# Performance work log

Measured on AMD Instinct MI355X. Metric: run time of the kernel, lower is better.

Reference implementation:

```python
import jax, jax.numpy as jnp
import numpy as np
from jax import lax

B, T_IN, T_OUT = 32, 256, 500
N_MEL, ENC_DIM = 80, 512
ATT_RNN, DEC_RNN, PRENET, ATT_DIM = 1024, 1024, 256, 128
LOC_F, LOC_K = 32, 31
P_ATT_DROP, P_DEC_DROP = 0.1, 0.1


def setup_inputs() -> dict:
    key = jax.random.key(0)
    ks = jax.random.split(key, 24)
    rn = lambda k, s, sc=0.02: jax.random.normal(k, s, dtype=jnp.float32) * sc
    inp = {}
    inp['memory'] = jax.random.normal(ks[0], (B, T_IN, ENC_DIM), dtype=jnp.float32)
    inp['decoder_inputs'] = jax.random.normal(ks[1], (B, N_MEL, T_OUT), dtype=jnp.float32)
    inp['memory_lengths'] = jax.random.randint(ks[2], (B,), T_IN // 2, T_IN + 1)
    inp['prenet_w1'] = rn(ks[3], (PRENET, N_MEL))
    inp['prenet_w2'] = rn(ks[4], (PRENET, PRENET))
    inp['att_w_ih'] = rn(ks[5], (4 * ATT_RNN, PRENET + ENC_DIM))
    inp['att_w_hh'] = rn(ks[6], (4 * ATT_RNN, ATT_RNN))
    inp['att_b_ih'] = jnp.zeros((4 * ATT_RNN,), jnp.float32)
    inp['att_b_hh'] = jnp.zeros((4 * ATT_RNN,), jnp.float32)
    inp['query_w'] = rn(ks[7], (ATT_DIM, ATT_RNN))
    inp['memory_w'] = rn(ks[8], (ATT_DIM, ENC_DIM))
    inp['v_w'] = rn(ks[9], (1, ATT_DIM))
    inp['loc_conv_w'] = rn(ks[10], (LOC_F, 2, LOC_K))
    inp['loc_dense_w'] = rn(ks[11], (ATT_DIM, LOC_F))
    inp['dec_w_ih'] = rn(ks[12], (4 * DEC_RNN, ATT_RNN + ENC_DIM))
    inp['dec_w_hh'] = rn(ks[13], (4 * DEC_RNN, DEC_RNN))
    inp['dec_b_ih'] = jnp.zeros((4 * DEC_RNN,), jnp.float32)
    inp['dec_b_hh'] = jnp.zeros((4 * DEC_RNN,), jnp.float32)
    inp['proj_w'] = rn(ks[14], (N_MEL, DEC_RNN + ENC_DIM))
    inp['proj_b'] = jnp.zeros((N_MEL,), jnp.float32)
    inp['gate_w'] = rn(ks[15], (1, DEC_RNN + ENC_DIM))
    inp['gate_b'] = jnp.zeros((1,), jnp.float32)
    return inp


def _lstm_cell(x, h, c, w_ih, w_hh, b_ih, b_hh):
    gates = x @ w_ih.T + b_ih + h @ w_hh.T + b_hh
    i, f, g, o = jnp.split(gates, 4, axis=-1)
    c2 = jax.nn.sigmoid(f) * c + jax.nn.sigmoid(i) * jnp.tanh(g)
    h2 = jax.nn.sigmoid(o) * jnp.tanh(c2)
    return h2, c2


def _dropout_masks():
    # deterministic dropout masks (training=True semantics), keep-prob scaled
    kd = jax.random.key(1)
    k1, k2, k3, k4 = jax.random.split(kd, 4)
    m1 = jax.random.bernoulli(k1, 0.5, (T_OUT + 1, B, PRENET)).astype(jnp.float32) / 0.5
    m2 = jax.random.bernoulli(k2, 0.5, (T_OUT + 1, B, PRENET)).astype(jnp.float32) / 0.5
    ma = jax.random.bernoulli(k3, 1 - P_ATT_DROP, (T_OUT, B, ATT_RNN)).astype(jnp.float32) / (1 - P_ATT_DROP)
    md = jax.random.bernoulli(k4, 1 - P_DEC_DROP, (T_OUT, B, DEC_RNN)).astype(jnp.float32) / (1 - P_DEC_DROP)
    return m1, m2, ma, md


def _decode(memory, decoder_inputs, memory_lengths, prenet_w1, prenet_w2,
            att_w_ih, att_w_hh, att_b_ih, att_b_hh, query_w, memory_w, v_w,
            loc_conv_w, loc_dense_w, dec_w_ih, dec_w_hh, dec_b_ih, dec_b_hh,
            proj_w, proj_b, gate_w, gate_b):
    pm1, pm2, att_drop, dec_drop = _dropout_masks()
    processed_memory = jnp.einsum('bte,ae->bta', memory, memory_w)  # (B,T_in,128)
    pad_mask = jnp.arange(T_IN)[None, :] >= memory_lengths[:, None]  # True = padded

    # teacher-forced decoder inputs: (B,n_mel,T) -> (T,B,n_mel), prepend go frame
    dec_in = jnp.transpose(decoder_inputs, (2, 0, 1))
    dec_in = jnp.concatenate([jnp.zeros((1, B, N_MEL), dec_in.dtype), dec_in], 0)
    # prenet (relu + dropout p=0.5, always training)
    x = jax.nn.relu(dec_in @ prenet_w1.T) * pm1
    x = jax.nn.relu(x @ prenet_w2.T) * pm2
    prenet_out = x[:T_OUT]  # (T,B,256)

    pad = (LOC_K - 1) // 2

    def attention(att_h, aw, aw_cum):
        pq = att_h @ query_w.T  # (B,128)
        awc = jnp.stack([aw, aw_cum], axis=1)  # (B,2,T_in)
        loc = lax.conv_general_dilated(awc, loc_conv_w, (1,), [(pad, pad)],
                                       dimension_numbers=('NCH', 'OIH', 'NCH'))  # (B,32,T_in)
        loc = jnp.einsum('bft,af->bta', loc, loc_dense_w)  # (B,T_in,128)
        energies = jnp.tanh(pq[:, None, :] + loc + processed_memory) @ v_w[0]  # (B,T_in)
        energies = jnp.where(pad_mask, -jnp.inf, energies)
        w = jax.nn.softmax(energies, axis=1)
        ctx = jnp.einsum('bt,bte->be', w, memory)  # (B,512)
        return ctx, w

    def step(carry, xs):
        ah, ac, dh, dc, aw, aw_cum, ctx = carry
        pn, adm, ddm = xs
        cell_in = jnp.concatenate([pn, ctx], axis=-1)  # (B,768)
        ah, ac = _lstm_cell(cell_in, ah, ac, att_w_ih, att_w_hh, att_b_ih, att_b_hh)
        ah = ah * adm
        ctx, aw = attention(ah, aw, aw_cum)
        aw_cum = aw_cum + aw
        din = jnp.concatenate([ah, ctx], axis=-1)  # (B,1536)
        dh, dc = _lstm_cell(din, dh, dc, dec_w_ih, dec_w_hh, dec_b_ih, dec_b_hh)
        dh = dh * ddm
        dhac = jnp.concatenate([dh, ctx], axis=-1)  # (B,1536)
        mel = dhac @ proj_w.T + proj_b  # (B,80)
        gate = (dhac @ gate_w.T + gate_b)[:, 0]  # (B,)
        return (ah, ac, dh, dc, aw, aw_cum, ctx), (mel, gate, aw)

    z = lambda d: jnp.zeros((B, d), jnp.float32)
    init = (z(ATT_RNN), z(ATT_RNN), z(DEC_RNN), z(DEC_RNN),
            jnp.zeros((B, T_IN), jnp.float32), jnp.zeros((B, T_IN), jnp.float32), z(ENC_DIM))
    _, (mels, gates, aligns) = lax.scan(step, init, (prenet_out, att_drop, dec_drop))

    mel_outputs = jnp.transpose(mels, (1, 2, 0))   # (B, n_mel, T_out)
    gate_outputs = gates.T                          # (B, T_out)
    alignments = jnp.transpose(aligns, (1, 0, 2))   # (B, T_out, T_in)
    return mel_outputs, gate_outputs, alignments


def reference(memory, decoder_inputs, memory_lengths, prenet_w1, prenet_w2,
              att_w_ih, att_w_hh, att_b_ih, att_b_hh, query_w, memory_w, v_w,
              loc_conv_w, loc_dense_w, dec_w_ih, dec_w_hh, dec_b_ih, dec_b_hh,
              proj_w, proj_b, gate_w, gate_b):
    return _decode(memory, decoder_inputs, memory_lengths, prenet_w1, prenet_w2,
                   att_w_ih, att_w_hh, att_b_ih, att_b_hh, query_w, memory_w, v_w,
                   loc_conv_w, loc_dense_w, dec_w_ih, dec_w_hh, dec_b_ih, dec_b_hh,
                   proj_w, proj_b, gate_w, gate_b)
```

## Files before the change

kernel.cpp:

```cpp
#include <hip/hip_runtime.h>
#include <math.h>
#include <string.h>

#define TOUT 500
#define AOFF 1296000
#define GOFF 1280000
#define TF_BITS_XOR 1

typedef float f32x4 __attribute__((ext_vector_type(4)));
typedef short bf16x8 __attribute__((ext_vector_type(8)));
typedef unsigned short ushort4_t __attribute__((ext_vector_type(4)));
typedef unsigned u32x4 __attribute__((ext_vector_type(4)));

struct Params {
  const float *memory, *dec_in, *pw1, *pw2, *awih, *awhh, *abih, *abhh;
  const float *qw, *mw, *vw, *lcw, *ldw, *dwih, *dwhh, *dbih, *dbhh;
  const float *pjw, *pjb, *gw, *gb;
  const int* mlen;
  float* out;
  unsigned short *ahb0, *ahb1, *dhb0, *dhb1, *ctxb0, *ctxb1;
  unsigned *slots;
  unsigned *abf;
  unsigned *dbf;
  unsigned *attflag;
  unsigned *decflag;
  float *x1, *w1t, *w2t, *mwt, *ldwt, *ba, *bd;
  unsigned short *pre_bf, *pm_bf, *mem_t, *qw_bf, *wpa, *wpd;
  unsigned *mma, *mmd, *mm1, *mm2;
};

__host__ __device__ inline void tf_block(unsigned k0, unsigned k1, unsigned x0, unsigned x1,
                                         unsigned& o0, unsigned& o1) {
  unsigned ks2 = k0 ^ k1 ^ 0x1BD11BDAu;
  x0 += k0; x1 += k1;
#define TFR(r) { x0 += x1; x1 = (x1 << r) | (x1 >> (32 - r)); x1 ^= x0; }
  TFR(13) TFR(15) TFR(26) TFR(6)
  x0 += k1;  x1 += ks2 + 1u;
  TFR(17) TFR(29) TFR(16) TFR(24)
  x0 += ks2; x1 += k0 + 2u;
  TFR(13) TFR(15) TFR(26) TFR(6)
  x0 += k0;  x1 += k1 + 3u;
  TFR(17) TFR(29) TFR(16) TFR(24)
  x0 += k1;  x1 += ks2 + 4u;
  TFR(13) TFR(15) TFR(26) TFR(6)
  x0 += ks2; x1 += k0 + 5u;
#undef TFR
  o0 = x0; o1 = x1;
}

__device__ inline float sigf(float x) { return 1.f / (1.f + __expf(-x)); }
__device__ inline float tanh_fast(float x) {
  float ax = fabsf(x);
  float t = __expf(-2.f * ax);
  float r = (1.f - t) / (1.f + t);
  return copysignf(r, x);
}
__device__ inline unsigned short f2bf(float f) {
  unsigned u = __float_as_uint(f);
  unsigned r = (u + 0x7FFFu + ((u >> 16) & 1u)) >> 16;
  return (unsigned short)r;
}
__device__ inline float bf2f(unsigned short u) {
  return __uint_as_float((unsigned)u << 16);
}

__device__ inline unsigned long long ld_coh64(const void* ptr) {
  return __hip_atomic_load((unsigned long long*)ptr, __ATOMIC_RELAXED, __HIP_MEMORY_SCOPE_SYSTEM);
}
__device__ inline unsigned ld_coh32(const unsigned* ptr) {
  return __hip_atomic_load(ptr, __ATOMIC_RELAXED, __HIP_MEMORY_SCOPE_SYSTEM);
}
__device__ inline void st_coh32(unsigned* ptr, unsigned v) {
  __hip_atomic_store(ptr, v, __ATOMIC_RELAXED, __HIP_MEMORY_SCOPE_SYSTEM);
}

template<bool COH>
__device__ __forceinline__ u32x4 ld16(const void* ptr) {
  u32x4 r;
  if constexpr (COH)
    asm volatile("global_load_dwordx4 %0, %1, off sc0 sc1" : "=v"(r) : "v"(ptr));
  else
    asm volatile("global_load_dwordx4 %0, %1, off" : "=v"(r) : "v"(ptr));
  return r;
}

#define LD4(p) (*(const float4*)(p))

__global__ void maskgen_kernel(Params p, unsigned k1a, unsigned k1b, unsigned k2a, unsigned k2b,
                               unsigned k3a, unsigned k3b, unsigned k4a, unsigned k4b) {
  int t = blockIdx.x * 256 + threadIdx.x;
  unsigned ka, kb; unsigned* dst; float pp;
  if (t < 512000)       { ka = k3a; kb = k3b; dst = p.mma; pp = 0.9f; }
  else if (t < 1024000) { t -= 512000;  ka = k4a; kb = k4b; dst = p.mmd; pp = 0.9f; }
  else if (t < 1152256) { t -= 1024000; ka = k1a; kb = k1b; dst = p.mm1; pp = 0.5f; }
  else if (t < 1280512) { t -= 1152256; ka = k2a; kb = k2b; dst = p.mm2; pp = 0.5f; }
  else return;
  unsigned word = 0u;
  for (int i = 0; i < 32; ++i) {
    unsigned o0, o1;
    tf_block(ka, kb, 0u, (unsigned)t * 32u + (unsigned)i, o0, o1);
#if TF_BITS_XOR
    unsigned bits = o0 ^ o1;
#else
    unsigned bits = o0;
#endif
    unsigned fb = (bits >> 9) | 0x3f800000u;
    float u = __uint_as_float(fb) - 1.0f;
    if (u < pp) word |= (1u << i);
  }
  dst[t] = word;
}

__global__ void prep_misc(Params p) {
  int i = blockIdx.x * 256 + threadIdx.x;
  if (i < 20480) { int k = i >> 8, u = i & 255; p.w1t[i] = p.pw1[u * 80 + k]; return; }
  i -= 20480;
  if (i < 65536) { int k = i >> 8, u = i & 255; p.w2t[i] = p.pw2[u * 256 + k]; return; }
  i -= 65536;
  if (i < 65536) { int k = i >> 7, a = i & 127; p.mwt[i] = p.mw[a * 512 + k]; return; }
  i -= 65536;
  if (i < 131072) { p.qw_bf[i] = f2bf(p.qw[i]); return; }
  i -= 131072;
  if (i < 4096) { int f = i >> 7, a = i & 127; p.ldwt[i] = p.ldw[a * 32 + f]; return; }
  i -= 4096;
  if (i < 4096) { int col = (i & 3) * 1024 + (i >> 2); p.ba[i] = p.abih[col] + p.abhh[col]; return; }
  i -= 4096;
  if (i < 4096) { int col = (i & 3) * 1024 + (i >> 2); p.bd[i] = p.dbih[col] + p.dbhh[col]; return; }
  i -= 4096;
  if (i < 4194304) {
    int b = i >> 17, rem = i & 131071, d = rem >> 8, t = rem & 255;
    p.mem_t[i] = f2bf(p.memory[((size_t)b * 256 + t) * 512 + d]);
    return;
  }
}

__global__ void pack_att(Params p) {
  int idx = blockIdx.x * 256 + threadIdx.x;
  if (idx >= 256 * 56 * 64) return;
  int l = idx & 63;
  int c = (idx >> 6) % 56;
  int T = idx / (56 * 64);
  int n = T * 16 + (l & 15);
  int col = (n & 3) * 1024 + (n >> 2);
  int kb = c * 32 + 8 * (l >> 4);
  bf16x8 v;
#pragma unroll
  for (int j = 0; j < 8; ++j) {
    int k = kb + j;
    float f = (k < 768) ? p.awih[(size_t)col * 768 + k] : p.awhh[(size_t)col * 1024 + k - 768];
    v[j] = (short)f2bf(f);
  }
  *(bf16x8*)(p.wpa + (size_t)idx * 8) = v;
}
__global__ void pack_dec(Params p) {
  int idx = blockIdx.x * 256 + threadIdx.x;
  if (idx >= 256 * 80 * 64) return;
  int l = idx & 63;
  int c = (idx >> 6) % 80;
  int T = idx / (80 * 64);
  int n = T * 16 + (l & 15);
  int col = (n & 3) * 1024 + (n >> 2);
  int kb = c * 32 + 8 * (l >> 4);
  bf16x8 v;
#pragma unroll
  for (int j = 0; j < 8; ++j) {
    int k = kb + j;
    float f = (k < 1536) ? p.dwih[(size_t)col * 1536 + k] : p.dwhh[(size_t)col * 1024 + k - 1536];
    v[j] = (short)f2bf(f);
  }
  *(bf16x8*)(p.wpd + (size_t)idx * 8) = v;
}

__global__ void prenet1_kernel(Params p) {
  __shared__ float din[8][80];
  int wg = blockIdx.x, tid = threadIdx.x;
  int r0 = wg * 8;
  for (int idx = tid; idx < 8 * 80; idx += 256) {
    int j = idx / 80, kk = idx % 80;
    int r = r0 + j; int t = r >> 5, b = r & 31;
    din[j][kk] = (t == 0) ? 0.f : p.dec_in[(size_t)b * 40000 + (size_t)kk * 500 + (t - 1)];
  }
  __syncthreads();
  float acc[8] = {0,0,0,0,0,0,0,0};
  for (int k = 0; k < 80; ++k) {
    float wv = p.w1t[k * 256 + tid];
#pragma unroll
    for (int j = 0; j < 8; ++j) acc[j] += din[j][k] * wv;
  }
  for (int j = 0; j < 8; ++j) {
    int r = r0 + j;
    unsigned e = (unsigned)r * 256u + tid;
    float mv = ((p.mm1[e >> 5] >> (e & 31)) & 1u) ? 2.0f : 0.0f;
    p.x1[(size_t)r * 256 + tid] = fmaxf(acc[j], 0.f) * mv;
  }
}
__global__ void prenet2_kernel(Params p) {
  __shared__ float rows[8][256];
  int wg = blockIdx.x, tid = threadIdx.x;
  int r0 = wg * 8;
  for (int idx = tid; idx < 8 * 256; idx += 256) {
    int j = idx >> 8, kk = idx & 255;
    rows[j][kk] = p.x1[(size_t)(r0 + j) * 256 + kk];
  }
  __syncthreads();
  float acc[8] = {0,0,0,0,0,0,0,0};
  for (int k = 0; k < 256; ++k) {
    float wv = p.w2t[k * 256 + tid];
#pragma unroll
    for (int j = 0; j < 8; ++j) acc[j] += rows[j][k] * wv;
  }
  for (int j = 0; j < 8; ++j) {
    int r = r0 + j;
    unsigned e = (unsigned)r * 256u + tid;
    float mv = ((p.mm2[e >> 5] >> (e & 31)) & 1u) ? 2.0f : 0.0f;
    p.pre_bf[(size_t)r * 256 + tid] = f2bf(fmaxf(acc[j], 0.f) * mv);
  }
}

__global__ void pm_kernel(Params p) {
  __shared__ float mrows[16][512];
  int wg = blockIdx.x;
  int b = wg >> 4, tc = wg & 15;
  int tid = threadIdx.x;
  int t0 = tc * 16;
  for (int idx = tid; idx < 16 * 512; idx += 128) {
    int i = idx >> 9, k = idx & 511;
    mrows[i][k] = p.memory[((size_t)b * 256 + t0 + i) * 512 + k];
  }
  __syncthreads();
  float acc[16];
#pragma unroll
  for (int i = 0; i < 16; ++i) acc[i] = 0.f;
  for (int k = 0; k < 512; ++k) {
    float wv = p.mwt[k * 128 + tid];
#pragma unroll
    for (int i = 0; i < 16; ++i) acc[i] += mrows[i][k] * wv;
  }
  for (int i = 0; i < 16; ++i)
    p.pm_bf[((size_t)b * 256 + t0 + i) * 128 + tid] = f2bf(acc[i]);
}

template<int LEN, bool COH>
struct Seg {
  static constexpr int CPR = LEN / 8;
  static constexpr int N = (32 * CPR) / 512;
  u32x4 r[N];
  __device__ __forceinline__ void load(const unsigned short* src, int srcStride, int tid) {
#pragma unroll
    for (int i = 0; i < N; ++i) {
      int idx = tid + i * 512;
      int b = idx / CPR, c = idx % CPR;
      r[i] = ld16<COH>(src + (size_t)b * srcStride + c * 8);
    }
  }
  __device__ __forceinline__ void store(unsigned short* dst, int dstOff, int dstStride, int tid) {
#pragma unroll
    for (int i = 0; i < N; ++i) {
      int idx = tid + i * 512;
      int b = idx / CPR, c = idx % CPR;
      *(u32x4*)(dst + b * dstStride + dstOff + c * 8) = r[i];
    }
  }
};

__device__ __forceinline__ void drain_vm() {
  asm volatile("s_waitcnt vmcnt(0)" ::: "memory");
  __builtin_amdgcn_sched_barrier(0);
}

#define MFMA_BF16(a, b, c) __builtin_amdgcn_mfma_f32_16x16x32_bf16(a, b, c, 0, 0, 0)

template<int NC, int CPW, int P0J, bool ATT>
__device__ __forceinline__ void gemm_tile2(const Params& p, const bf16x8* bfa, const bf16x8* bfb,
                                           int lane, int v, int s,
                                           const unsigned short* ctxb_in,
                                           const unsigned short* ahb_in,
                                           const unsigned short* dhb_in,
                                           unsigned short* Abuf, float* pl, int tid) {
  const int arow = lane & 15;
  const int kgrp = (lane >> 4) * 8;
  f32x4 acc00 = {0,0,0,0}, acc01 = {0,0,0,0}, acc10 = {0,0,0,0}, acc11 = {0,0,0,0};

  const int RS0 = ATT ? 776 : 1288;
  if (ATT) {
    Seg<256, false> s0; Seg<512, true> s1;
    s0.load(p.pre_bf + (size_t)s * 32 * 256, 256, tid);
    s1.load(ctxb_in, 512, tid);
    drain_vm();
    s0.store(Abuf, 0, RS0, tid);
    s1.store(Abuf, 256, RS0, tid);
  } else {
    Seg<1024, true> s0; Seg<256, true> s1;
    s0.load(ahb_in, 1024, tid);
    s1.load(ctxb_in, 512, tid);
    drain_vm();
    s0.store(Abuf, 0, RS0, tid);
    s1.store(Abuf, 1024, RS0, tid);
  }
  __syncthreads();
#pragma unroll
  for (int j = 0; j < P0J; ++j) {
    const int kc = (v + 8 * j) * 32;
    const int off = arow * RS0 + kc + kgrp;
    bf16x8 a0 = *(const bf16x8*)&Abuf[off];
    bf16x8 a1 = *(const bf16x8*)&Abuf[off + 16 * RS0];
    acc00 = MFMA_BF16(a0, bfa[j], acc00);
    acc01 = MFMA_BF16(a1, bfa[j], acc01);
    acc10 = MFMA_BF16(a0, bfb[j], acc10);
    acc11 = MFMA_BF16(a1, bfb[j], acc11);
  }
  __syncthreads();

  const int RS1 = ATT ? 1032 : 1288;
  if (ATT) {
    Seg<1024, true> s0;
    s0.load(ahb_in, 1024, tid);
    drain_vm();
    s0.store(Abuf, 0, RS1, tid);
  } else {
    Seg<256, true> s0; Seg<1024, true> s1;
    s0.load(ctxb_in + 256, 512, tid);
    s1.load(dhb_in, 1024, tid);
    drain_vm();
    s0.store(Abuf, 0, RS1, tid);
    s1.store(Abuf, 256, RS1, tid);
  }
  __syncthreads();
  const int K1 = ATT ? 768 : 1280;
#pragma unroll
  for (int j = P0J; j < CPW; ++j) {
    const int kc = (v + 8 * j) * 32 - K1;
    const int off = arow * RS1 + kc + kgrp;
    bf16x8 a0 = *(const bf16x8*)&Abuf[off];
    bf16x8 a1 = *(const bf16x8*)&Abuf[off + 16 * RS1];
    acc00 = MFMA_BF16(a0, bfa[j], acc00);
    acc01 = MFMA_BF16(a1, bfa[j], acc01);
    acc10 = MFMA_BF16(a0, bfb[j], acc10);
    acc11 = MFMA_BF16(a1, bfb[j], acc11);
  }
  __syncthreads();

  const int po = (lane & 15) * 17 + (lane >> 4) * 4;
#pragma unroll
  for (int j = 0; j < 4; ++j) {
    pl[v * 1088 +   0 + po + j] = acc00[j];
    pl[v * 1088 + 272 + po + j] = acc01[j];
    pl[v * 1088 + 544 + po + j] = acc10[j];
    pl[v * 1088 + 816 + po + j] = acc11[j];
  }
}

template<bool ATT>
__device__ __forceinline__ void lstm_tail(const Params& p, int wgl, int tid, unsigned step,
                                          unsigned short* hout, float* pl, float* gates,
                                          float* cst, unsigned short* hst) {
  __syncthreads();
  {
    const float* bias = ATT ? p.ba : p.bd;
    const int nb32 = wgl * 32;
#pragma unroll
    for (int rep = 0; rep < 2; ++rep) {
      int o = rep * 512 + tid;
      int tile = o >> 9, half = (o >> 8) & 1, n = (o >> 4) & 15, brow = o & 15;
      int o2 = (tile * 2 + half) * 272 + n * 17 + brow;
      float acc = 0.f;
#pragma unroll
      for (int w = 0; w < 8; ++w) acc += pl[w * 1088 + o2];
      int n_local = tile * 16 + n;
      gates[n_local * 33 + half * 16 + brow] = acc + bias[nb32 + n_local];
    }
  }
  __syncthreads();
  if (tid < 256) {
    int u_local = tid >> 5, b = tid & 31;
    float gi = gates[(u_local * 4 + 0) * 33 + b];
    float gf = gates[(u_local * 4 + 1) * 33 + b];
    float gg = gates[(u_local * 4 + 2) * 33 + b];
    float go = gates[(u_local * 4 + 3) * 33 + b];
    float I = sigf(gi), F = sigf(gf), G = tanh_fast(gg), O = sigf(go);
    float c2 = F * cst[tid] + I * G;
    float h = O * tanh_fast(c2);
    cst[tid] = c2;
    int u = wgl * 8 + u_local;
    const unsigned* maskw = ATT ? p.mma : p.mmd;
    unsigned e = (step * 32 + (unsigned)b) * 1024u + (unsigned)u;
    float mv = ((maskw[e >> 5] >> (e & 31)) & 1u) ? (1.f / 0.9f) : 0.f;
    hst[tid] = f2bf(h * mv);
  }
  __syncthreads();
  if (tid < 128) {
    int j = tid >> 5, bb = tid & 31;
    unsigned lo = hst[j * 64 + bb], hi = hst[j * 64 + 32 + bb];
    unsigned val = lo | (hi << 16);
    int T8 = wgl * 8;
    st_coh32((unsigned*)(hout + (size_t)bb * 1024 + T8 + 2 * j), val);
  }
}

template<bool MASTER>
__device__ __forceinline__ void dbar(const Params& p, unsigned* flg, int base, int wg, int tid, unsigned gen) {
  __syncthreads();
  if (MASTER) {
    if (tid == 0) st_coh32(p.slots + (base + (wg & 127)) * 32, gen);
    for (;;) {
      int ok = 1;
      if (tid < 128) ok = (ld_coh32(p.slots + (base + tid) * 32) >= gen) ? 1 : 0;
      if (__syncthreads_count(ok) == 512) break;
      __builtin_amdgcn_s_sleep(1);
    }
    if (tid < 8) st_coh32(flg + tid * 32, gen);
  } else {
    if (tid == 0) {
      st_coh32(p.slots + (base + (wg & 127)) * 32, gen);
      while (ld_coh32(flg + (wg & 7) * 32) < gen)
        __builtin_amdgcn_s_sleep(2);
    }
    __syncthreads();
  }
}

template<bool MASTER>
__device__ void run_att(const Params& p, int wg, int tid,
                        unsigned short* Abuf, float* pl, float* gates,
                        float* cst, float* aw_l, float* awc_l, float* sm,
                        unsigned short* ahst, unsigned short* cxst, unsigned short* hst) {
  const int lane = tid & 63;
  const int v = tid >> 6;
  const int Tb = wg * 2;

  bf16x8 bfa[7], bfb[7];
#pragma unroll
  for (int j = 0; j < 7; ++j) {
    const int c = v + 8 * j;
    const unsigned short* bp = p.wpa + ((size_t)(Tb * 56 + c) * 64 + lane) * 8;
    bfa[j] = *(const bf16x8*)bp;
    bfb[j] = *(const bf16x8*)(bp + (size_t)56 * 64 * 8);
  }

  unsigned gen = 0;
  for (int s = 0; s < 500; ++s) {
    const int sb = s & 1;
    const unsigned short* ahb_prev = sb ? p.ahb0 : p.ahb1;
    unsigned short*       ahb_cur  = sb ? p.ahb1 : p.ahb0;
    const unsigned short* ctxb_prev = sb ? p.ctxb0 : p.ctxb1;
    unsigned short*       ctxb_cur  = sb ? p.ctxb1 : p.ctxb0;

    if (tid == 0) {
      while ((int)ld_coh32(p.decflag + (wg & 7) * 32) < s - 1)
        __builtin_amdgcn_s_sleep(4);
    }
    __syncthreads();

    gemm_tile2<56, 7, 3, true>(p, bfa, bfb, lane, v, s, ctxb_prev, ahb_prev, nullptr, Abuf, pl, tid);
    lstm_tail<true>(p, wg, tid, (unsigned)s, ahb_cur, pl, gates, cst, hst);

    dbar<MASTER>(p, p.abf, 0, wg, tid, ++gen);

    if (wg < 32) {
      const int b = wg;
      unsigned short* locT_bf = (unsigned short*)pl;
      float* ldwt_l = (float*)((char*)(void*)pl + 16640);
      {
        const float4* srcw = (const float4*)p.ldwt;
        float4* dstw = (float4*)ldwt_l;
        dstw[tid] = srcw[tid];
        dstw[tid + 512] = srcw[tid + 512];
      }
      if (tid < 256) {
        unsigned long long q = ld_coh64((const unsigned long long*)(ahb_cur + (size_t)b * 1024) + tid);
        *(unsigned long long*)&ahst[tid * 4] = q;
      }
#pragma unroll
      for (int rep = 0; rep < 4; ++rep) {
        int qd = rep * 512 + tid;
        int f = qd >> 6, tq = (qd & 63) * 4;
        const float* wf = p.lcw + f * 62;
        float w[36]; float acc[4] = {0, 0, 0, 0};
#pragma unroll
        for (int j2 = 0; j2 < 9; ++j2) {
          float4 x = *(const float4*)&aw_l[tq + j2 * 4];
          w[j2*4] = x.x; w[j2*4+1] = x.y; w[j2*4+2] = x.z; w[j2*4+3] = x.w;
        }
#pragma unroll
        for (int k = 0; k < 31; ++k) {
          float cc = wf[k];
          acc[0] += w[k+1]*cc; acc[1] += w[k+2]*cc; acc[2] += w[k+3]*cc; acc[3] += w[k+4]*cc;
        }
#pragma unroll
        for (int j2 = 0; j2 < 9; ++j2) {
          float4 x = *(const float4*)&awc_l[tq + j2 * 4];
          w[j2*4] = x.x; w[j2*4+1] = x.y; w[j2*4+2] = x.z; w[j2*4+3] = x.w;
        }
#pragma unroll
        for (int k = 0; k < 31; ++k) {
          float cc = wf[31 + k];
          acc[0] += w[k+1]*cc; acc[1] += w[k+2]*cc; acc[2] += w[k+3]*cc; acc[3] += w[k+4]*cc;
        }
#pragma unroll
        for (int j2 = 0; j2 < 4; ++j2) locT_bf[f * 260 + tq + j2] = f2bf(acc[j2]);
      }
      __syncthreads();
      {
        int a = tid & 127, kq = tid >> 7;
        const unsigned short* qp = p.qw_bf + (size_t)a * 1024 + kq * 256;
        float acc = 0.f;
#pragma unroll 4
        for (int j = 0; j < 256; j += 8) {
          bf16x8 qv = *(const bf16x8*)(qp + j);
          bf16x8 av = *(const bf16x8*)&ahst[kq * 256 + j];
#pragma unroll
          for (int j2 = 0; j2 < 8; ++j2)
            acc += bf2f((unsigned short)av[j2]) * bf2f((unsigned short)qv[j2]);
        }
        sm[256 + kq * 128 + a] = acc;
        if (tid < 128) sm[128 + tid] = p.vw[tid];
      }
      __syncthreads();
      if (tid < 128) sm[tid] = sm[256 + tid] + sm[384 + tid] + sm[512 + tid] + sm[640 + tid];
      __syncthreads();
      {
        int t = tid & 255, h2 = tid >> 8;
        float lt[32];
#pragma unroll
        for (int f = 0; f < 32; ++f) lt[f] = bf2f(locT_bf[f * 260 + t]);
        const unsigned short* pmp = p.pm_bf + ((size_t)b * 256 + t) * 128;
        float e = 0.f;
#pragma unroll 2
        for (int ac = 0; ac < 16; ++ac) {
          int a0 = h2 * 64 + ac * 4;
          float4 l2 = {0, 0, 0, 0};
#pragma unroll
          for (int f = 0; f < 32; ++f) {
            float4 wv = *(const float4*)&ldwt_l[f * 128 + a0];
            l2.x += lt[f]*wv.x; l2.y += lt[f]*wv.y; l2.z += lt[f]*wv.z; l2.w += lt[f]*wv.w;
          }
          ushort4_t pv = *(const ushort4_t*)(pmp + a0);
          e += tanh_fast(sm[a0+0] + l2.x + bf2f(pv.x)) * sm[128+a0+0];
          e += tanh_fast(sm[a0+1] + l2.y + bf2f(pv.y)) * sm[128+a0+1];
          e += tanh_fast(sm[a0+2] + l2.z + bf2f(pv.z)) * sm[128+a0+2];
          e += tanh_fast(sm[a0+3] + l2.w + bf2f(pv.w)) * sm[128+a0+3];
        }
        sm[256 + h2 * 256 + t] = e;
      }
      __syncthreads();
      if (tid < 256) {
        float en = sm[256 + tid] + sm[512 + tid];
        float w = (tid < p.mlen[b]) ? __expf(en) : 0.f;
        sm[768 + tid] = w;
      }
      __syncthreads();
      if (tid < 32) {
        float sub = 0.f;
#pragma unroll
        for (int i2 = 0; i2 < 8; ++i2) sub += sm[768 + tid * 8 + i2];
        sm[256 + tid] = sub;
      }
      __syncthreads();
      if (tid == 0) {
        float S = 0.f;
#pragma unroll
        for (int i2 = 0; i2 < 32; ++i2) S += sm[256 + i2];
        sm[1281] = 1.f / S;
      }
      __syncthreads();
      if (tid < 256) {
        float awv = sm[768 + tid] * sm[1281];
        aw_l[16 + tid] = awv;
        awc_l[16 + tid] += awv;
        p.out[(size_t)AOFF + (size_t)b * 128000 + (size_t)s * 256 + tid] = awv;
        sm[1024 + tid] = awv;
      }
      __syncthreads();
      {
        const unsigned short* mt = p.mem_t + (size_t)b * 131072 + (size_t)tid * 256;
        float acc = 0.f;
#pragma unroll 8
        for (int t2 = 0; t2 < 256; t2 += 8) {
          bf16x8 mv = *(const bf16x8*)(mt + t2);
#pragma unroll
          for (int j2 = 0; j2 < 8; ++j2)
            acc += sm[1024 + t2 + j2] * bf2f((unsigned short)mv[j2]);
        }
        cxst[tid] = f2bf(acc);
      }
      __syncthreads();
      if (tid < 256) {
        unsigned val = (unsigned)cxst[2 * tid] | ((unsigned)cxst[2 * tid + 1] << 16);
        st_coh32((unsigned*)(ctxb_cur + (size_t)b * 512 + 2 * tid), val);
      }
    }

    dbar<MASTER>(p, p.abf, 0, wg, tid, ++gen);

    if (MASTER && tid < 8) st_coh32(p.attflag + tid * 32, (unsigned)(s + 1));
  }
}

template<bool MASTER>
__device__ void run_dec(const Params& p, int wg, int tid,
                        unsigned short* Abuf, float* pl, float* gates,
                        float* cst, float* sm, unsigned short* ahst, unsigned short* hst) {
  const int lane = tid & 63;
  const int v = tid >> 6;
  const int wgl = wg - 128;
  const int Tb = wgl * 2;

  bf16x8 bfa[10], bfb[10];
#pragma unroll
  for (int j = 0; j < 10; ++j) {
    const int c = v + 8 * j;
    const unsigned short* bp = p.wpd + ((size_t)(Tb * 80 + c) * 64 + lane) * 8;
    bfa[j] = *(const bf16x8*)bp;
    bfb[j] = *(const bf16x8*)(bp + (size_t)80 * 64 * 8);
  }
  const int melb = wgl >> 2, melc4 = wgl & 3;

  unsigned gen = 0;
  for (int i = 0; i < 500; ++i) {
    const int ib = i & 1;
    const unsigned short* ahb_i  = ib ? p.ahb1 : p.ahb0;
    const unsigned short* ctxb_i = ib ? p.ctxb1 : p.ctxb0;
    const unsigned short* dhb_prev = ib ? p.dhb0 : p.dhb1;
    unsigned short*       dhb_cur  = ib ? p.dhb1 : p.dhb0;

    if (tid == 0) {
      while ((int)ld_coh32(p.attflag + (wg & 7) * 32) < i + 1)
        __builtin_amdgcn_s_sleep(4);
    }
    __syncthreads();

    gemm_tile2<80, 10, 5, false>(p, bfa, bfb, lane, v, i, ctxb_i, ahb_i, dhb_prev, Abuf, pl, tid);
    lstm_tail<false>(p, wgl, tid, (unsigned)i, dhb_cur, pl, gates, cst, hst);

    dbar<MASTER>(p, p.dbf, 128, wg, tid, ++gen);

    {
      if (tid < 384) {
        unsigned long long q;
        if (tid < 256) q = ld_coh64((const unsigned long long*)(dhb_cur + (size_t)melb * 1024) + tid);
        else           q = ld_coh64((const unsigned long long*)(ctxb_i + (size_t)melb * 512) + (tid - 256));
        *(unsigned long long*)&ahst[tid * 4] = q;
      }
      __syncthreads();
      int mi = tid >> 5, kg = tid & 31;
#pragma unroll
      for (int rep = 0; rep < 2; ++rep) {
        int mm = rep * 16 + mi;
        if (mm < 20) {
          int m = melc4 * 20 + mm;
          const float* pw = p.pjw + (size_t)m * 1536 + kg * 48;
          float acc = 0.f;
#pragma unroll 4
          for (int j = 0; j < 48; ++j) acc += bf2f(ahst[kg * 48 + j]) * pw[j];
          sm[mm * 32 + kg] = acc;
        }
      }
      if (melc4 == 3 && tid >= 384) {
        int kg2 = tid - 384;
        const float* gwp = p.gw + kg2 * 12;
        float acc = 0.f;
#pragma unroll
        for (int j = 0; j < 12; ++j) acc += bf2f(ahst[kg2 * 12 + j]) * gwp[j];
        sm[896 + kg2] = acc;
      }
      __syncthreads();
      if (tid < 20) {
        float r = p.pjb[melc4 * 20 + tid];
#pragma unroll
        for (int j = 0; j < 32; ++j) r += sm[tid * 32 + j];
        p.out[(size_t)melb * 40000 + (size_t)(melc4 * 20 + tid) * 500 + i] = r;
      }
      if (melc4 == 3 && tid == 384) {
        float r = p.gb[0];
#pragma unroll
        for (int j = 0; j < 128; ++j) r += sm[896 + j];
        p.out[(size_t)GOFF + (size_t)melb * 500 + i] = r;
      }
    }

    dbar<MASTER>(p, p.dbf, 128, wg, tid, ++gen);

    if (MASTER && tid < 8) st_coh32(p.decflag + tid * 32, (unsigned)(i + 1));
  }
}

__global__ void __launch_bounds__(512, 1) scan_kernel(Params p) {
  const int wg = blockIdx.x;
  const int tid = threadIdx.x;

  __shared__ __align__(16) unsigned short Abuf[32 * 1288];
  float* pl = (float*)Abuf;
  __shared__ float gates[32 * 33];
  __shared__ float cst[256];
  __shared__ float aw_l[292], awc_l[292];
  __shared__ float sm[1536];
  __shared__ unsigned short ahst[1536];
  __shared__ unsigned short cxst[512];
  __shared__ unsigned short hst[256];

  if (tid < 256) cst[tid] = 0.f;
  if (tid < 292) { aw_l[tid] = 0.f; awc_l[tid] = 0.f; }

  if (wg < 128) {
    if (wg == 32) run_att<true >(p, wg, tid, Abuf, pl, gates, cst, aw_l, awc_l, sm, ahst, cxst, hst);
    else          run_att<false>(p, wg, tid, Abuf, pl, gates, cst, aw_l, awc_l, sm, ahst, cxst, hst);
  } else {
    if (wg == 160) run_dec<true >(p, wg, tid, Abuf, pl, gates, cst, sm, ahst, hst);
    else           run_dec<false>(p, wg, tid, Abuf, pl, gates, cst, sm, ahst, hst);
  }
}

extern "C" void kernel_launch(void* const* d_in, const int* in_sizes, int n_in,
                              void* d_out, int out_size, void* d_ws, size_t ws_size,
                              hipStream_t stream) {
  Params p;
  p.memory = (const float*)d_in[0];
  p.dec_in = (const float*)d_in[1];
  p.mlen   = (const int*)d_in[2];
  p.pw1  = (const float*)d_in[3];
  p.pw2  = (const float*)d_in[4];
  p.awih = (const float*)d_in[5];
  p.awhh = (const float*)d_in[6];
  p.abih = (const float*)d_in[7];
  p.abhh = (const float*)d_in[8];
  p.qw   = (const float*)d_in[9];
  p.mw   = (const float*)d_in[10];
  p.vw   = (const float*)d_in[11];
  p.lcw  = (const float*)d_in[12];
  p.ldw  = (const float*)d_in[13];
  p.dwih = (const float*)d_in[14];
  p.dwhh = (const float*)d_in[15];
  p.dbih = (const float*)d_in[16];
  p.dbhh = (const float*)d_in[17];
  p.pjw  = (const float*)d_in[18];
  p.pjb  = (const float*)d_in[19];
  p.gw   = (const float*)d_in[20];
  p.gb   = (const float*)d_in[21];
  p.out  = (float*)d_out;

  char* cur = (char*)d_ws;
  auto allocf = [&](size_t n) { float* r = (float*)cur; cur += n * sizeof(float); return r; };
  auto allocs = [&](size_t n) { unsigned short* r = (unsigned short*)cur; cur += n * sizeof(unsigned short); return r; };
  p.ahb0 = allocs(32 * 1024); p.ahb1 = allocs(32 * 1024);
  p.dhb0 = allocs(32 * 1024); p.dhb1 = allocs(32 * 1024);
  p.ctxb0 = allocs(32 * 512); p.ctxb1 = allocs(32 * 512);
  p.slots   = (unsigned*)cur; cur += 256 * 32 * sizeof(unsigned);
  p.abf     = (unsigned*)cur; cur += 8 * 32 * sizeof(unsigned);
  p.dbf     = (unsigned*)cur; cur += 8 * 32 * sizeof(unsigned);
  p.attflag = (unsigned*)cur; cur += 8 * 32 * sizeof(unsigned);
  p.decflag = (unsigned*)cur; cur += 8 * 32 * sizeof(unsigned);
  size_t state_bytes = (size_t)(cur - (char*)d_ws);
  p.x1   = allocf((size_t)500 * 32 * 256);
  p.w1t  = allocf(80 * 256);
  p.w2t  = allocf(256 * 256);
  p.mwt  = allocf(512 * 128);
  p.ldwt = allocf(32 * 128);
  p.ba   = allocf(4096);
  p.bd   = allocf(4096);
  p.pre_bf  = allocs((size_t)500 * 32 * 256);
  p.pm_bf   = allocs((size_t)32 * 256 * 128);
  p.mem_t   = allocs((size_t)32 * 512 * 256);
  p.qw_bf   = allocs(128 * 1024);
  p.wpa     = allocs((size_t)256 * 56 * 64 * 8);
  p.wpd     = allocs((size_t)256 * 80 * 64 * 8);
  p.mma = (unsigned*)cur; cur += 512000u * 4;
  p.mmd = (unsigned*)cur; cur += 512000u * 4;
  p.mm1 = (unsigned*)cur; cur += 128256u * 4;
  p.mm2 = (unsigned*)cur; cur += 128256u * 4;

  (void)hipMemsetAsync(d_ws, 0, state_bytes, stream);

  unsigned k[8];
  {
    unsigned o0, o1;
    tf_block(0u, 1u, 0u, 0u, o0, o1); k[0] = o0; k[1] = o1;
    tf_block(0u, 1u, 0u, 1u, o0, o1); k[2] = o0; k[3] = o1;
    tf_block(0u, 1u, 0u, 2u, o0, o1); k[4] = o0; k[5] = o1;
    tf_block(0u, 1u, 0u, 3u, o0, o1); k[6] = o0; k[7] = o1;
  }

  maskgen_kernel<<<(1280512 + 255) / 256, 256, 0, stream>>>(p, k[0], k[1], k[2], k[3], k[4], k[5], k[6], k[7]);
  prep_misc<<<(4489216 + 255) / 256, 256, 0, stream>>>(p);
  pack_att<<<(917504 + 255) / 256, 256, 0, stream>>>(p);
  pack_dec<<<(1310720 + 255) / 256, 256, 0, stream>>>(p);
  prenet1_kernel<<<2000, 256, 0, stream>>>(p);
  prenet2_kernel<<<2000, 256, 0, stream>>>(p);
  pm_kernel<<<512, 128, 0, stream>>>(p);

  void* args[] = { (void*)&p };
  (void)hipLaunchCooperativeKernel((const void*)scan_kernel, dim3(256), dim3(512), args, 0, stream);
}
```

Measured before the change: 34.77 ms.

## Replace system-coherent loads with sc0 loads plus per-XCD one-shot cache invalidation

Cross-workgroup state loads switch from system-scope coherent loads (sc0 sc1) and atomic 64-bit loads to sc0-only loads. Correctness is kept by a per-XCD claim/done protocol: after each grid barrier or flag wait, one workgroup per XCD issues an agent-scope acquire fence, which invalidates that XCD's L2, and the others wait for it. The aim is to stop every load of shared hidden state from bypassing the caches, so that reads of ahb, dhb and ctx buffers can hit in L2. In exchange each barrier gains an extra atomic step and a wait, and correctness now depends on how XCD L2 coherence behaves.

```diff
diff --git a/kernel.cpp b/kernel.cpp
--- a/kernel.cpp
+++ b/kernel.cpp
@@ -24,6 +24,9 @@
   unsigned *dbf;
   unsigned *attflag;
   unsigned *decflag;
+  unsigned *clA, *dnA;
+  unsigned *clD, *dnD;
+  unsigned *clW, *dnW;
   float *x1, *w1t, *w2t, *mwt, *ldwt, *ba, *bd;
   unsigned short *pre_bf, *pm_bf, *mem_t, *qw_bf, *wpa, *wpd;
   unsigned *mma, *mmd, *mm1, *mm2;
@@ -64,9 +67,6 @@
   return __uint_as_float((unsigned)u << 16);
 }
 
-__device__ inline unsigned long long ld_coh64(const void* ptr) {
-  return __hip_atomic_load((unsigned long long*)ptr, __ATOMIC_RELAXED, __HIP_MEMORY_SCOPE_SYSTEM);
-}
 __device__ inline unsigned ld_coh32(const unsigned* ptr) {
   return __hip_atomic_load(ptr, __ATOMIC_RELAXED, __HIP_MEMORY_SCOPE_SYSTEM);
 }
@@ -74,14 +74,42 @@
   __hip_atomic_store(ptr, v, __ATOMIC_RELAXED, __HIP_MEMORY_SCOPE_SYSTEM);
 }
 
-template<bool COH>
-__device__ __forceinline__ u32x4 ld16(const void* ptr) {
+__device__ __forceinline__ u32x4 ld16_sc0(const void* ptr) {
   u32x4 r;
-  if constexpr (COH)
-    asm volatile("global_load_dwordx4 %0, %1, off sc0 sc1" : "=v"(r) : "v"(ptr));
-  else
-    asm volatile("global_load_dwordx4 %0, %1, off" : "=v"(r) : "v"(ptr));
+  asm volatile("global_load_dwordx4 %0, %1, off sc0" : "=v"(r) : "v"(ptr));
   return r;
+}
+__device__ __forceinline__ u32x4 ld16_plain(const void* ptr) {
+  u32x4 r;
+  asm volatile("global_load_dwordx4 %0, %1, off" : "=v"(r) : "v"(ptr));
+  return r;
+}
+__device__ __forceinline__ unsigned long long ld8_sc0(const void* ptr) {
+  unsigned long long r;
+  asm volatile("global_load_dwordx2 %0, %1, off sc0" : "=v"(r) : "v"(ptr));
+  return r;
+}
+
+__device__ __forceinline__ void drain_vm() {
+  asm volatile("s_waitcnt vmcnt(0)" ::: "memory");
+  __builtin_amdgcn_sched_barrier(0);
+}
+
+__device__ __forceinline__ int get_xcd() {
+  unsigned x;
+  asm volatile("s_getreg_b32 %0, hwreg(HW_REG_XCC_ID)" : "=s"(x));
+  return (int)(x & 7);
+}
+
+__device__ __forceinline__ void inv_once(unsigned* claim, unsigned* done, int xcd, unsigned gen) {
+  unsigned old = __hip_atomic_fetch_max(claim + xcd * 32, gen, __ATOMIC_RELAXED, __HIP_MEMORY_SCOPE_SYSTEM);
+  if (old < gen) {
+    __builtin_amdgcn_fence(__ATOMIC_ACQUIRE, "agent");
+    st_coh32(done + xcd * 32, gen);
+  } else {
+    while (ld_coh32(done + xcd * 32) < gen)
+      __builtin_amdgcn_s_sleep(1);
+  }
 }
 
 #define LD4(p) (*(const float4*)(p))
@@ -250,7 +278,8 @@
     for (int i = 0; i < N; ++i) {
       int idx = tid + i * 512;
       int b = idx / CPR, c = idx % CPR;
-      r[i] = ld16<COH>(src + (size_t)b * srcStride + c * 8);
+      if (COH) r[i] = ld16_sc0(src + (size_t)b * srcStride + c * 8);
+      else     r[i] = ld16_plain(src + (size_t)b * srcStride + c * 8);
     }
   }
   __device__ __forceinline__ void store(unsigned short* dst, int dstOff, int dstStride, int tid) {
@@ -262,11 +291,6 @@
     }
   }
 };
-
-__device__ __forceinline__ void drain_vm() {
-  asm volatile("s_waitcnt vmcnt(0)" ::: "memory");
-  __builtin_amdgcn_sched_barrier(0);
-}
 
 #define MFMA_BF16(a, b, c) __builtin_amdgcn_mfma_f32_16x16x32_bf16(a, b, c, 0, 0, 0)
 
@@ -398,7 +422,8 @@
 }
 
 template<bool MASTER>
-__device__ __forceinline__ void dbar(const Params& p, unsigned* flg, int base, int wg, int tid, unsigned gen) {
+__device__ __forceinline__ void dbar(const Params& p, unsigned* flg, unsigned* cl, unsigned* dn,
+                                     int base, int wg, int tid, int xcd, unsigned gen) {
   __syncthreads();
   if (MASTER) {
     if (tid == 0) st_coh32(p.slots + (base + (wg & 127)) * 32, gen);
@@ -409,11 +434,14 @@
       __builtin_amdgcn_s_sleep(1);
     }
     if (tid < 8) st_coh32(flg + tid * 32, gen);
+    if (tid == 0) inv_once(cl, dn, xcd, gen);
+    __syncthreads();
   } else {
     if (tid == 0) {
       st_coh32(p.slots + (base + (wg & 127)) * 32, gen);
       while (ld_coh32(flg + (wg & 7) * 32) < gen)
         __builtin_amdgcn_s_sleep(2);
+      inv_once(cl, dn, xcd, gen);
     }
     __syncthreads();
   }
@@ -427,6 +455,7 @@
   const int lane = tid & 63;
   const int v = tid >> 6;
   const int Tb = wg * 2;
+  const int xcd = get_xcd();
 
   bf16x8 bfa[7], bfb[7];
 #pragma unroll
@@ -454,7 +483,7 @@
     gemm_tile2<56, 7, 3, true>(p, bfa, bfb, lane, v, s, ctxb_prev, ahb_prev, nullptr, Abuf, pl, tid);
     lstm_tail<true>(p, wg, tid, (unsigned)s, ahb_cur, pl, gates, cst, hst);
 
-    dbar<MASTER>(p, p.abf, 0, wg, tid, ++gen);
+    dbar<MASTER>(p, p.abf, p.clA, p.dnA, 0, wg, tid, xcd, ++gen);
 
     if (wg < 32) {
       const int b = wg;
@@ -466,10 +495,10 @@
         dstw[tid] = srcw[tid];
         dstw[tid + 512] = srcw[tid + 512];
       }
-      if (tid < 256) {
-        unsigned long long q = ld_coh64((const unsigned long long*)(ahb_cur + (size_t)b * 1024) + tid);
-        *(unsigned long long*)&ahst[tid * 4] = q;
-      }
+      unsigned long long q0 = 0;
+      if (tid < 256) q0 = ld8_sc0((const unsigned long long*)(ahb_cur + (size_t)b * 1024) + tid);
+      drain_vm();
+      if (tid < 256) *(unsigned long long*)&ahst[tid * 4] = q0;
 #pragma unroll
       for (int rep = 0; rep < 4; ++rep) {
         int qd = rep * 512 + tid;
@@ -590,7 +619,7 @@
       }
     }
 
-    dbar<MASTER>(p, p.abf, 0, wg, tid, ++gen);
+    dbar<MASTER>(p, p.abf, p.clA, p.dnA, 0, wg, tid, xcd, ++gen);
 
     if (MASTER && tid < 8) st_coh32(p.attflag + tid * 32, (unsigned)(s + 1));
   }
@@ -604,6 +633,7 @@
   const int v = tid >> 6;
   const int wgl = wg - 128;
   const int Tb = wgl * 2;
+  const int xcd = get_xcd();
 
   bf16x8 bfa[10], bfb[10];
 #pragma unroll
@@ -626,21 +656,23 @@
     if (tid == 0) {
       while ((int)ld_coh32(p.attflag + (wg & 7) * 32) < i + 1)
         __builtin_amdgcn_s_sleep(4);
+      inv_once(p.clW, p.dnW, xcd, (unsigned)(i + 1));
     }
     __syncthreads();
 
     gemm_tile2<80, 10, 5, false>(p, bfa, bfb, lane, v, i, ctxb_i, ahb_i, dhb_prev, Abuf, pl, tid);
     lstm_tail<false>(p, wgl, tid, (unsigned)i, dhb_cur, pl, gates, cst, hst);
 
-    dbar<MASTER>(p, p.dbf, 128, wg, tid, ++gen);
+    dbar<MASTER>(p, p.dbf, p.clD, p.dnD, 128, wg, tid, xcd, ++gen);
 
     {
+      unsigned long long q0 = 0;
       if (tid < 384) {
-        unsigned long long q;
-        if (tid < 256) q = ld_coh64((const unsigned long long*)(dhb_cur + (size_t)melb * 1024) + tid);
-        else           q = ld_coh64((const unsigned long long*)(ctxb_i + (size_t)melb * 512) + (tid - 256));
-        *(unsigned long long*)&ahst[tid * 4] = q;
-      }
+        if (tid < 256) q0 = ld8_sc0((const unsigned long long*)(dhb_cur + (size_t)melb * 1024) + tid);
+        else           q0 = ld8_sc0((const unsigned long long*)(ctxb_i + (size_t)melb * 512) + (tid - 256));
+      }
+      drain_vm();
+      if (tid < 384) *(unsigned long long*)&ahst[tid * 4] = q0;
       __syncthreads();
       int mi = tid >> 5, kg = tid & 31;
 #pragma unroll
@@ -678,7 +710,7 @@
       }
     }
 
-    dbar<MASTER>(p, p.dbf, 128, wg, tid, ++gen);
+    dbar<MASTER>(p, p.dbf, p.clD, p.dnD, 128, wg, tid, xcd, ++gen);
 
     if (MASTER && tid < 8) st_coh32(p.decflag + tid * 32, (unsigned)(i + 1));
   }
@@ -741,14 +773,18 @@
   char* cur = (char*)d_ws;
   auto allocf = [&](size_t n) { float* r = (float*)cur; cur += n * sizeof(float); return r; };
   auto allocs = [&](size_t n) { unsigned short* r = (unsigned short*)cur; cur += n * sizeof(unsigned short); return r; };
+  auto allocu = [&](size_t n) { unsigned* r = (unsigned*)cur; cur += n * sizeof(unsigned); return r; };
   p.ahb0 = allocs(32 * 1024); p.ahb1 = allocs(32 * 1024);
   p.dhb0 = allocs(32 * 1024); p.dhb1 = allocs(32 * 1024);
   p.ctxb0 = allocs(32 * 512); p.ctxb1 = allocs(32 * 512);
-  p.slots   = (unsigned*)cur; cur += 256 * 32 * sizeof(unsigned);
-  p.abf     = (unsigned*)cur; cur += 8 * 32 * sizeof(unsigned);
-  p.dbf     = (unsigned*)cur; cur += 8 * 32 * sizeof(unsigned);
-  p.attflag = (unsigned*)cur; cur += 8 * 32 * sizeof(unsigned);
-  p.decflag = (unsigned*)cur; cur += 8 * 32 * sizeof(unsigned);
+  p.slots   = allocu(256 * 32);
+  p.abf     = allocu(8 * 32);
+  p.dbf     = allocu(8 * 32);
+  p.attflag = allocu(8 * 32);
+  p.decflag = allocu(8 * 32);
+  p.clA = allocu(8 * 32); p.dnA = allocu(8 * 32);
+  p.clD = allocu(8 * 32); p.dnD = allocu(8 * 32);
+  p.clW = allocu(8 * 32); p.dnW = allocu(8 * 32);
   size_t state_bytes = (size_t)(cur - (char*)d_ws);
   p.x1   = allocf((size_t)500 * 32 * 256);
   p.w1t  = allocf(80 * 256);
```

After: 35.49 ms. 1.02x slower.
